# Performance work log

Measured on AMD Instinct MI355X. Metric: run time of the kernel, lower is better.

Reference implementation:

```python
import jax, jax.numpy as jnp
import numpy as np


def setup_inputs() -> dict:
    key = jax.random.key(0)
    kx, kw = jax.random.split(key)
    x = jax.random.normal(kx, (32, 256, 56, 56), dtype=jnp.float32)
    weight = jax.random.uniform(kw, (256, 256, 3, 3), dtype=jnp.float32) * 0.001
    return {"x": x, "weight": weight}


def reference(x, weight):
    # --- binarize activations with straight-through estimator ---
    # forward value = sign(x); gradient flows through clamp(x, -1, 1)
    clipped_x = jnp.clip(x, -1.0, 1.0)
    bx = jax.lax.stop_gradient(jnp.sign(x) - clipped_x) + clipped_x

    # --- binarize weights (per-output-channel mean-centered, scaled sign) ---
    w = weight
    # subtract per-output-channel mean over (in_c, kh, kw)
    bw = w - jnp.mean(w.reshape(w.shape[0], -1), axis=-1)[:, None, None, None]
    # per-output-channel scaling factor = mean |bw| (detached)
    scale = jnp.mean(jnp.abs(bw), axis=(1, 2, 3), keepdims=True)
    scale = jax.lax.stop_gradient(scale)
    clipped_w = jnp.clip(bw, -1.0, 1.0)
    binary_w = jax.lax.stop_gradient(scale * jnp.sign(bw) - clipped_w) + clipped_w

    # --- conv2d, NCHW / OIHW, stride 1, padding 1 ---
    y = jax.lax.conv_general_dilated(
        bx, binary_w,
        window_strides=(1, 1),
        padding=((1, 1), (1, 1)),
        dimension_numbers=("NCHW", "OIHW", "NCHW"),
    )
    return y
```

## Files before the change

kernel.cpp:

```cpp
#include <hip/hip_runtime.h>
#include <cstdint>
#include <cstddef>

#define N_ 32
#define C_ 256
#define H_ 56
#define W_ 56

typedef int v4i __attribute__((ext_vector_type(4)));

static constexpr size_t WB_BYTES = 36ull * 16 * 64 * 16;
static constexpr size_t SC_OFF   = WB_BYTES;

__device__ __forceinline__ uint32_t sgnw(uint32_t u) {
    return (u & 0x7fffffffu) ? (((uint32_t)(((int)u) >> 31) | 1u) & 0xffu) : 0u;
}
__device__ __forceinline__ uint32_t sgnb(uint32_t u) {
    return ((uint32_t)(((int)u) >> 31) | 1u) & 0xffu;
}
__device__ __forceinline__ uint32_t pack4f(float4 v) {
    return sgnb(__float_as_uint(v.x)) | (sgnb(__float_as_uint(v.y)) << 8) |
           (sgnb(__float_as_uint(v.z)) << 16) | (sgnb(__float_as_uint(v.w)) << 24);
}

__global__ __launch_bounds__(256) void pack_w(const float* __restrict__ wt,
                                              char* __restrict__ wB,
                                              float* __restrict__ scaleg) {
    __shared__ double red[256];
    int o = blockIdx.x, tid = threadIdx.x;
    const float* wo = wt + (size_t)o * 2304;

    double s = 0;
    for (int j = tid; j < 2304; j += 256) s += (double)wo[j];
    red[tid] = s;
    __syncthreads();
    for (int k = 128; k > 0; k >>= 1) {
        if (tid < k) red[tid] += red[tid + k];
        __syncthreads();
    }
    double mean = red[0] / 2304.0;
    __syncthreads();

    double s2 = 0;
    for (int j = tid; j < 2304; j += 256) s2 += fabs((double)wo[j] - mean);
    red[tid] = s2;
    __syncthreads();
    for (int k = 128; k > 0; k >>= 1) {
        if (tid < k) red[tid] += red[tid + k];
        __syncthreads();
    }
    if (tid == 0) scaleg[o] = (float)(red[0] / 2304.0);

    if (tid < 144) {
        int kiter = tid >> 2, q = tid & 3;
        int tap = kiter >> 2, cb = kiter & 3;
        int kh = tap / 3, kw = tap - kh * 3;
        int words[4];
        for (int g = 0; g < 4; ++g) {
            int word = 0;
            for (int b = 0; b < 4; ++b) {
                int c = cb * 64 + q * 16 + g * 4 + b;
                double v = (double)wo[c * 9 + kh * 3 + kw];
                int sg = (v > mean) - (v < mean);
                word |= (sg & 0xff) << (8 * b);
            }
            words[g] = word;
        }
        v4i pk = {words[0], words[1], words[2], words[3]};
        *(v4i*)(wB + (((size_t)kiter * 16 + (o >> 4)) * 64 + q * 16 + (o & 15)) * 16) = pk;
    }
}

__global__ __launch_bounds__(256, 2) void conv_mfma(const float* __restrict__ x,
                                                    const v4i* __restrict__ wB,
                                                    const float* __restrict__ scaleg,
                                                    float* __restrict__ out) {
    __shared__ char xs[4 * 58 * 256];
    int tid = threadIdx.x;
    int wave = tid >> 6, lane = tid & 63;

    int lin = blockIdx.x + 14 * blockIdx.y;
    int swz = (lin & 7) * 56 + (lin >> 3);
    int hq = swz % 14, n = swz / 14;
    int h0a = hq * 4;

    auto unit = [&](int ir0, int u) {
        int R   = u / 224;
        int rem = u - R * 224;
        int ch  = rem / 14;
        int wq  = rem - ch * 14;
        int ir  = ir0 + R;
        int slot = ir & 3;
        if (ir < 0 || ir > 55) {
            v4i z = {0, 0, 0, 0};
#pragma unroll
            for (int h = 0; h < 4; ++h) {
                int wp = 1 + wq * 4 + h;
                int s16 = (ch + wp) & 15;
                *(v4i*)(xs + ((size_t)(slot * 58 + wp) << 8) + (s16 << 4)) = z;
            }
            return;
        }
        const float* xb = x + ((size_t)n * C_ + ch * 16) * 3136 + ir * 56 + wq * 4;
        uint32_t sw[16];
#pragma unroll
        for (int c = 0; c < 16; ++c)
            sw[c] = pack4f(*(const float4*)(xb + (size_t)c * 3136));
        uint32_t t[4][4];
#pragma unroll
        for (int p = 0; p < 4; ++p) {
            uint32_t lo01 = __builtin_amdgcn_perm(sw[4*p+1], sw[4*p+0], 0x05010400u);
            uint32_t hi01 = __builtin_amdgcn_perm(sw[4*p+1], sw[4*p+0], 0x07030602u);
            uint32_t lo23 = __builtin_amdgcn_perm(sw[4*p+3], sw[4*p+2], 0x05010400u);
            uint32_t hi23 = __builtin_amdgcn_perm(sw[4*p+3], sw[4*p+2], 0x07030602u);
            t[p][0] = __builtin_amdgcn_perm(lo23, lo01, 0x05040100u);
            t[p][1] = __builtin_amdgcn_perm(lo23, lo01, 0x07060302u);
            t[p][2] = __builtin_amdgcn_perm(hi23, hi01, 0x05040100u);
            t[p][3] = __builtin_amdgcn_perm(hi23, hi01, 0x07060302u);
        }
#pragma unroll
        for (int h = 0; h < 4; ++h) {
            int wp = 1 + wq * 4 + h;
            int s16 = (ch + wp) & 15;
            v4i c4 = {(int)t[0][h], (int)t[1][h], (int)t[2][h], (int)t[3][h]};
            *(v4i*)(xs + ((size_t)(slot * 58 + wp) << 8) + (s16 << 4)) = c4;
        }
    };
    auto halo = [&](int ir0, int u) {
        int r  = u >> 5;
        int c2 = u & 31;
        int slot = (ir0 + r) & 3;
        int wp = (c2 >> 4) * 57;
        int ch = c2 & 15;
        int s16 = (ch + wp) & 15;
        v4i z = {0, 0, 0, 0};
        *(v4i*)(xs + ((size_t)(slot * 58 + wp) << 8) + (s16 << 4)) = z;
    };

    if (tid < 128) halo(h0a - 1, tid);
    unit(h0a - 1, tid);
    unit(h0a - 1, tid + 256);
    unit(h0a - 1, tid + 512);
    if (tid < 128) unit(h0a - 1, tid + 768);

    int lm = lane & 15, q = lane >> 4;
    int og = wave;
    int kstart = __builtin_amdgcn_readfirstlane(wave * 9);

    int wof[7], ro[7], slotb[7];
#pragma unroll
    for (int mf = 0; mf < 7; ++mf) {
        int m = mf * 16 + lm;
        int r = m / 56;
        ro[mf]    = r;
        wof[mf]   = m - r * 56;
        slotb[mf] = q + wof[mf];
    }

    const v4i* wBw = wB + (size_t)(og * 4) * 64 + lane;

    auto wrap = [&](int t) {
        int k = kstart + t;
        if (k >= 36) k -= 36;
        if (k >= 36) k -= 36;
        return k;
    };
    auto loadB = [&](int k, v4i (&b)[4]) {
#pragma unroll
        for (int of = 0; of < 4; ++of) b[of] = wBw[(size_t)k * 1024 + of * 64];
    };

    auto run_iter = [&](int h0it) {
        v4i acc[7][4];
#pragma unroll
        for (int mf = 0; mf < 7; ++mf)
#pragma unroll
            for (int of = 0; of < 4; ++of) { v4i z = {0, 0, 0, 0}; acc[mf][of] = z; }

        v4i bR0[4], bR1[4], bR2[4];
        loadB(wrap(0), bR0);
        loadB(wrap(1), bR1);
        loadB(wrap(2), bR2);

        auto step = [&](v4i (&bReg)[4], int t) {
            int k = wrap(t);
            int tap = k >> 2, cb = k & 3;
            int dh = (tap * 11) >> 5;
            int dw = tap - dh * 3;
            int s0 = (h0it - 1 + dh) & 3;
            int s1 = (s0 + 1) & 3;
            int p0 = s0 * 58 + dw;
            int dpr = (s1 - s0) * 58;
            int sofs = cb * 4 + dw;
            v4i a[7];
#pragma unroll
            for (int mf = 0; mf < 7; ++mf) {
                int pos = p0 + ro[mf] * dpr + wof[mf];
                int s16 = (slotb[mf] + sofs) & 15;
                a[mf] = *(const v4i*)(xs + ((size_t)pos << 8) + (s16 << 4));
            }
            __builtin_amdgcn_s_setprio(1);
#pragma unroll
            for (int mf = 0; mf < 7; ++mf)
#pragma unroll
                for (int of = 0; of < 4; ++of)
                    acc[mf][of] = __builtin_amdgcn_mfma_i32_16x16x64_i8(
                        a[mf], bReg[of], acc[mf][of], 0, 0, 0);
            __builtin_amdgcn_s_setprio(0);
            loadB(wrap(t + 3), bReg);
        };

        for (int t3 = 0; t3 < 12; ++t3) {
            int t = t3 * 3;
            step(bR0, t);
            step(bR1, t + 1);
            step(bR2, t + 2);
        }

#pragma unroll
        for (int of = 0; of < 4; ++of) {
            int o = (og * 4 + of) * 16 + lm;
            float s = scaleg[o];
#pragma unroll
            for (int mf = 0; mf < 7; ++mf) {
                int m  = mf * 16 + q * 4;
                int r  = m / 56;
                int wb = m - r * 56;
                float* ob = out + ((size_t)(n * C_ + o) * H_ + h0it + r) * W_ + wb;
                float4 v = {s * (float)acc[mf][of].x, s * (float)acc[mf][of].y,
                            s * (float)acc[mf][of].z, s * (float)acc[mf][of].w};
                *(float4*)ob = v;
            }
        }
    };

    __syncthreads();
    run_iter(h0a);

    __syncthreads();
    if (tid < 64) halo(h0a + 3, tid);
    unit(h0a + 3, tid);
    if (tid < 192) unit(h0a + 3, tid + 256);
    __syncthreads();

    run_iter(h0a + 2);
}

extern "C" void kernel_launch(void* const* d_in, const int* in_sizes, int n_in,
                              void* d_out, int out_size, void* d_ws, size_t ws_size,
                              hipStream_t stream) {
    const float* x   = (const float*)d_in[0];
    const float* wgt = (const float*)d_in[1];
    float* out = (float*)d_out;
    char* ws = (char*)d_ws;

    char*  wb = ws;
    float* sg = (float*)(ws + SC_OFF);

    pack_w<<<dim3(256), dim3(256), 0, stream>>>(wgt, wb, sg);
    conv_mfma<<<dim3(14, N_), dim3(256), 0, stream>>>(x, (const v4i*)wb, sg, out);
}
```

Baseline: 239.7 us.

## Rebalance grid into mixed 4-row and 3-row tiles to fill all CU slots

Replaces the 14x32 grid of uniform 4-row tiles with 512 blocks: half compute 4 output rows and half compute 3 rows, with the second pass of the 3-row blocks using a smaller templated fragment count. This is meant to spread the work evenly across all CUs at two blocks per CU instead of leaving some CUs with double load. It adds a branch and some wasted MFMA work in the partial 4-fragment pass.

Measured after the change: 247.9 us. +3.4%, slower.

```diff
diff --git a/kernel.cpp b/kernel.cpp
--- a/kernel.cpp
+++ b/kernel.cpp
@@ -8,6 +8,8 @@
 #define W_ 56
 
 typedef int v4i __attribute__((ext_vector_type(4)));
+
+template<int V> struct IC { static constexpr int value = V; };
 
 static constexpr size_t WB_BYTES = 36ull * 16 * 64 * 16;
 static constexpr size_t SC_OFF   = WB_BYTES;
@@ -79,14 +81,17 @@
     int tid = threadIdx.x;
     int wave = tid >> 6, lane = tid & 63;
 
-    int lin = blockIdx.x + 14 * blockIdx.y;
-    int swz = (lin & 7) * 56 + (lin >> 3);
-    int hq = swz % 14, n = swz / 14;
-    int h0a = hq * 4;
-
-    auto unit = [&](int ir0, int u) {
-        int R   = u / 224;
-        int rem = u - R * 224;
+    int b = blockIdx.x;
+    bool four = (b < 256);
+    int u = four ? b : b - 256;
+    int tile = (u & 7) * 32 + (u >> 3);
+    int n = tile >> 3;
+    int j = tile & 7;
+    int h0a = four ? j * 4 : 32 + j * 3;
+
+    auto unit = [&](int ir0, int uu) {
+        int R   = uu / 224;
+        int rem = uu - R * 224;
         int ch  = rem / 14;
         int wq  = rem - ch * 14;
         int ir  = ir0 + R;
@@ -126,9 +131,9 @@
             *(v4i*)(xs + ((size_t)(slot * 58 + wp) << 8) + (s16 << 4)) = c4;
         }
     };
-    auto halo = [&](int ir0, int u) {
-        int r  = u >> 5;
-        int c2 = u & 31;
+    auto halo = [&](int ir0, int uu) {
+        int r  = uu >> 5;
+        int c2 = uu & 31;
         int slot = (ir0 + r) & 3;
         int wp = (c2 >> 4) * 57;
         int ch = c2 & 15;
@@ -165,15 +170,16 @@
         if (k >= 36) k -= 36;
         return k;
     };
-    auto loadB = [&](int k, v4i (&b)[4]) {
-#pragma unroll
-        for (int of = 0; of < 4; ++of) b[of] = wBw[(size_t)k * 1024 + of * 64];
-    };
-
-    auto run_iter = [&](int h0it) {
-        v4i acc[7][4];
-#pragma unroll
-        for (int mf = 0; mf < 7; ++mf)
+    auto loadB = [&](int k, v4i (&bb)[4]) {
+#pragma unroll
+        for (int of = 0; of < 4; ++of) bb[of] = wBw[(size_t)k * 1024 + of * 64];
+    };
+
+    auto run_iter = [&](int h0it, auto NMFC) {
+        constexpr int NMF = decltype(NMFC)::value;
+        v4i acc[NMF][4];
+#pragma unroll
+        for (int mf = 0; mf < NMF; ++mf)
 #pragma unroll
             for (int of = 0; of < 4; ++of) { v4i z = {0, 0, 0, 0}; acc[mf][of] = z; }
 
@@ -192,16 +198,16 @@
             int p0 = s0 * 58 + dw;
             int dpr = (s1 - s0) * 58;
             int sofs = cb * 4 + dw;
-            v4i a[7];
-#pragma unroll
-            for (int mf = 0; mf < 7; ++mf) {
+            v4i a[NMF];
+#pragma unroll
+            for (int mf = 0; mf < NMF; ++mf) {
                 int pos = p0 + ro[mf] * dpr + wof[mf];
                 int s16 = (slotb[mf] + sofs) & 15;
                 a[mf] = *(const v4i*)(xs + ((size_t)pos << 8) + (s16 << 4));
             }
             __builtin_amdgcn_s_setprio(1);
 #pragma unroll
-            for (int mf = 0; mf < 7; ++mf)
+            for (int mf = 0; mf < NMF; ++mf)
 #pragma unroll
                 for (int of = 0; of < 4; ++of)
                     acc[mf][of] = __builtin_amdgcn_mfma_i32_16x16x64_i8(
@@ -222,8 +228,9 @@
             int o = (og * 4 + of) * 16 + lm;
             float s = scaleg[o];
 #pragma unroll
-            for (int mf = 0; mf < 7; ++mf) {
+            for (int mf = 0; mf < NMF; ++mf) {
                 int m  = mf * 16 + q * 4;
+                if (NMF == 4 && m >= 56) continue;
                 int r  = m / 56;
                 int wb = m - r * 56;
                 float* ob = out + ((size_t)(n * C_ + o) * H_ + h0it + r) * W_ + wb;
@@ -235,15 +242,21 @@
     };
 
     __syncthreads();
-    run_iter(h0a);
-
-    __syncthreads();
-    if (tid < 64) halo(h0a + 3, tid);
-    unit(h0a + 3, tid);
-    if (tid < 192) unit(h0a + 3, tid + 256);
-    __syncthreads();
-
-    run_iter(h0a + 2);
+    run_iter(h0a, IC<7>{});
+
+    __syncthreads();
+    if (four) {
+        if (tid < 64) halo(h0a + 3, tid);
+        unit(h0a + 3, tid);
+        if (tid < 192) unit(h0a + 3, tid + 256);
+        __syncthreads();
+        run_iter(h0a + 2, IC<7>{});
+    } else {
+        if (tid < 32) halo(h0a + 3, tid);
+        if (tid < 224) unit(h0a + 3, tid);
+        __syncthreads();
+        run_iter(h0a + 2, IC<4>{});
+    }
 }
 
 extern "C" void kernel_launch(void* const* d_in, const int* in_sizes, int n_in,
@@ -258,5 +271,5 @@
     float* sg = (float*)(ws + SC_OFF);
 
     pack_w<<<dim3(256), dim3(256), 0, stream>>>(wgt, wb, sg);
-    conv_mfma<<<dim3(14, N_), dim3(256), 0, stream>>>(x, (const v4i*)wb, sg, out);
-}
+    conv_mfma<<<dim3(512), dim3(256), 0, stream>>>(x, (const v4i*)wb, sg, out);
+}
```
